# Optimization experiments

Measured on AMD Instinct MI355X. Metric: run time of the kernel, lower is better.

Reference implementation:

```python
import jax, jax.numpy as jnp
import numpy as np

NUM_CIRCLES = 7
B, D_IN, D_HID, D_OUT = 4096, 2048, 3584, 2048  # D_HID % 7 == 0 (7 * 512)


def setup_inputs() -> dict:
    key = jax.random.key(0)
    k1, k2, k3, k4 = jax.random.split(key, 4)
    x = jax.random.normal(k1, (B, D_IN), dtype=jnp.float32)
    # FlowerOfLife: 7 bias-free Linear(D_IN -> D_HID//7) weights, stacked [7, D_HID//7, D_IN]
    W_flower = jax.random.normal(k2, (NUM_CIRCLES, D_HID // NUM_CIRCLES, D_IN), dtype=jnp.float32) / np.sqrt(D_IN).astype(np.float32)
    # Merkaba: two bias-free Linear(D_HID -> D_OUT)
    W_male = jax.random.normal(k3, (D_OUT, D_HID), dtype=jnp.float32) / np.sqrt(D_HID).astype(np.float32)
    W_female = jax.random.normal(k4, (D_OUT, D_HID), dtype=jnp.float32) / np.sqrt(D_HID).astype(np.float32)
    return {"x": x, "W_flower": W_flower, "W_male": W_male, "W_female": W_female}


def reference(x, W_flower, W_male, W_female):
    # --- VesicaPiscisOperation: sacred overlap with the batch-rolled neighbor ---
    x2 = jnp.roll(x, 1, axis=0)
    dist = jnp.linalg.norm(x - x2, axis=1, keepdims=True)          # [B, 1]
    overlap = jax.nn.relu(1.0 - jnp.abs(dist - 1.0))               # [B, 1]
    x_overlap = x * (1.0 + overlap)                                # per-row scaling

    # --- FlowerOfLifeProjection: 7 parallel projections, phase-shift first 2 dims ---
    circ = jnp.einsum('bd,cod->bco', x_overlap, W_flower)          # [B, 7, D_HID//7]
    phases = 2.0 * jnp.pi * jnp.arange(NUM_CIRCLES, dtype=jnp.float32) / NUM_CIRCLES
    phase_shift = jnp.stack([jnp.cos(phases), jnp.sin(phases)], axis=-1)  # [7, 2]
    circ = circ.at[:, :, :2].multiply(phase_shift[None, :, :])
    x_expanded = circ.reshape(x.shape[0], -1)                      # [B, D_HID]

    # --- MerkabaRotation: counter-rotating transforms + sigmoid phase lock ---
    male = x_expanded @ W_male.T                                   # [B, D_OUT]
    female = x_expanded[:, ::-1] @ W_female.T                      # flip(-1) then Linear
    phase_lock = jax.nn.sigmoid(jnp.sum(male * female, axis=-1, keepdims=True))
    return phase_lock * male + (1.0 - phase_lock) * female
```

## Files before the change

### kernel.cpp

```cpp
#include <hip/hip_runtime.h>
#include <hip/hip_bf16.h>
#include <math.h>

#define B_DIM 4096
#define D_IN  2048
#define D_HID 3584
#define D_OUT 2048

typedef __bf16 bf16;
typedef float  floatx4 __attribute__((ext_vector_type(4)));
typedef bf16   bf16x8  __attribute__((ext_vector_type(8)));
typedef bf16   bf16x4  __attribute__((ext_vector_type(4)));

typedef __attribute__((address_space(1))) const void* gptr1;
typedef __attribute__((address_space(3))) void*       lptr3;

__device__ __forceinline__ void load_lds16(const void* g, void* l) {
    __builtin_amdgcn_global_load_lds((gptr1)g, (lptr3)l, 16, 0, 0);
}

struct HL { bf16 h, l; };
__device__ __forceinline__ HL split2(float v) {
    HL r;
    r.h = (bf16)v;
    r.l = (bf16)(v - (float)r.h);
    return r;
}

__global__ __launch_bounds__(256) void vesica_kernel(const float* __restrict__ x,
                                                     bf16* __restrict__ xh,
                                                     bf16* __restrict__ xl) {
    const int b  = blockIdx.x;
    const int bp = (b == 0) ? (B_DIM - 1) : (b - 1);
    const int t  = threadIdx.x;

    const floatx4* xr = (const floatx4*)(x + (size_t)b  * D_IN);
    const floatx4* pr = (const floatx4*)(x + (size_t)bp * D_IN);
    const floatx4 v0 = xr[t * 2], v1 = xr[t * 2 + 1];
    const floatx4 p0 = pr[t * 2], p1 = pr[t * 2 + 1];

    float s = 0.f;
#pragma unroll
    for (int j = 0; j < 4; ++j) {
        const float d0 = v0[j] - p0[j], d1 = v1[j] - p1[j];
        s += d0 * d0 + d1 * d1;
    }
#pragma unroll
    for (int off = 32; off > 0; off >>= 1) s += __shfl_down(s, off, 64);

    __shared__ float red[4];
    const int wave = t >> 6, lane = t & 63;
    if (lane == 0) red[wave] = s;
    __syncthreads();
    const float dist = sqrtf(red[0] + red[1] + red[2] + red[3]);
    const float sc   = 1.f + fmaxf(0.f, 1.f - fabsf(dist - 1.f));

    bf16x8 h, l;
#pragma unroll
    for (int j = 0; j < 4; ++j) {
        const HL a  = split2(v0[j] * sc);
        const HL b2 = split2(v1[j] * sc);
        h[j] = a.h;      l[j] = a.l;
        h[4 + j] = b2.h; l[4 + j] = b2.l;
    }
    ((bf16x8*)(xh + (size_t)b * D_IN))[t] = h;
    ((bf16x8*)(xl + (size_t)b * D_IN))[t] = l;
}

__global__ __launch_bounds__(256) void split_kernel(const float* __restrict__ w,
                                                    bf16* __restrict__ wh,
                                                    bf16* __restrict__ wl) {
    const size_t i = (size_t)blockIdx.x * 256 + threadIdx.x;
    const floatx4 a = ((const floatx4*)w)[i * 2];
    const floatx4 b = ((const floatx4*)w)[i * 2 + 1];
    bf16x8 h, l;
#pragma unroll
    for (int j = 0; j < 4; ++j) {
        const HL u = split2(a[j]);
        const HL v = split2(b[j]);
        h[j] = u.h;     l[j] = u.l;
        h[4 + j] = v.h; l[4 + j] = v.l;
    }
    ((bf16x8*)wh)[i] = h;
    ((bf16x8*)wl)[i] = l;
}

__global__ __launch_bounds__(256) void flipsplit_kernel(const float* __restrict__ w,
                                                        bf16* __restrict__ wh,
                                                        bf16* __restrict__ wl) {
    const int i = blockIdx.x * 256 + threadIdx.x;
    const int o = i / 448;
    const int g = i - o * 448;
    const float* src = w + (size_t)o * 3584 + (size_t)(447 - g) * 8;
    const floatx4 a = ((const floatx4*)src)[0];
    const floatx4 b = ((const floatx4*)src)[1];
    bf16x8 h, l;
#pragma unroll
    for (int j = 0; j < 4; ++j) {
        const HL u = split2(b[3 - j]);
        const HL v = split2(a[3 - j]);
        h[j] = u.h;     l[j] = u.l;
        h[4 + j] = v.h; l[4 + j] = v.l;
    }
    ((bf16x8*)wh)[(size_t)o * 448 + g] = h;
    ((bf16x8*)wl)[(size_t)o * 448 + g] = l;
}

__global__ __launch_bounds__(256) void tsplit_kernel(const float* __restrict__ w,
                                                     bf16* __restrict__ th,
                                                     bf16* __restrict__ tl) {
    __shared__ float tile[64][65];
    const int d0 = blockIdx.x * 64;
    const int h0 = blockIdx.y * 64;
    const int t  = threadIdx.x;
    const int r  = t >> 4;
    const int cg = (t & 15) << 2;

#pragma unroll
    for (int i = 0; i < 4; ++i) {
        const int hr = r + i * 16;
        const floatx4 v = *(const floatx4*)&w[(size_t)(h0 + hr) * 2048 + d0 + cg];
        tile[hr][cg]     = v[0];
        tile[hr][cg + 1] = v[1];
        tile[hr][cg + 2] = v[2];
        tile[hr][cg + 3] = v[3];
    }
    __syncthreads();

    float pm[4];
#pragma unroll
    for (int j = 0; j < 4; ++j) {
        const int h  = h0 + cg + j;
        const int hm = h & 511;
        float p = 1.f;
        if (hm < 2) {
            const float ph = 0.8975979010256552f * (float)(h >> 9);
            p = (hm == 0) ? cosf(ph) : sinf(ph);
        }
        pm[j] = p;
    }

#pragma unroll
    for (int i = 0; i < 4; ++i) {
        const int dr = r + i * 16;
        bf16x4 hh, ll;
#pragma unroll
        for (int j = 0; j < 4; ++j) {
            const HL u = split2(tile[cg + j][dr] * pm[j]);
            hh[j] = u.h;
            ll[j] = u.l;
        }
        const size_t o = (size_t)(d0 + dr) * 3584 + h0 + cg;
        *(bf16x4*)&th[o] = hh;
        *(bf16x4*)&tl[o] = ll;
    }
}

__global__ __launch_bounds__(256, 2) void gemm3_single(const bf16* __restrict__ Ah,
                                                       const bf16* __restrict__ Al,
                                                       const bf16* __restrict__ Bh,
                                                       const bf16* __restrict__ Bl,
                                                       bf16* __restrict__ C0,
                                                       bf16* __restrict__ C1,
                                                       int M, int N, int K) {
    __shared__ bf16 sAh[128 * 64], sAl[128 * 64];
    __shared__ bf16 sBh[128 * 64], sBl[128 * 64];

    const int tid  = threadIdx.x;
    const int wave = tid >> 6;
    const int lane = tid & 63;
    const int m0   = blockIdx.y * 128;
    const int n0   = blockIdx.x * 128;
    const int wm   = wave & 1;
    const int wn   = wave >> 1;

    floatx4 acc[4][4];
#pragma unroll
    for (int i = 0; i < 4; ++i)
#pragma unroll
        for (int j = 0; j < 4; ++j) acc[i][j] = (floatx4){0.f, 0.f, 0.f, 0.f};

    const int lr  = lane & 15;
    const int cc8 = (lane >> 4) << 3;

    for (int kt = 0; kt < K; kt += 64) {
#pragma unroll
        for (int i = 0; i < 4; ++i) {
            const int q = ((i * 4 + wave) << 6) + lane;
            const int r = q >> 3, c = q & 7, e = q << 3;
            const size_t ga = (size_t)(m0 + r) * K + kt + c * 8;
            const size_t gb = (size_t)(n0 + r) * K + kt + c * 8;
            load_lds16(&Ah[ga], &sAh[e]);
            load_lds16(&Al[ga], &sAl[e]);
            load_lds16(&Bh[gb], &sBh[e]);
            load_lds16(&Bl[gb], &sBl[e]);
        }
        __syncthreads();

#pragma unroll
        for (int ks = 0; ks < 2; ++ks) {
            const int ko = (ks << 5) + cc8;
            bf16x8 ah[4], al[4], bh[4], bl[4];
#pragma unroll
            for (int mi = 0; mi < 4; ++mi) {
                const int off = ((wm * 64 + mi * 16 + lr) << 6) + ko;
                ah[mi] = *(const bf16x8*)&sAh[off];
                al[mi] = *(const bf16x8*)&sAl[off];
            }
#pragma unroll
            for (int ni = 0; ni < 4; ++ni) {
                const int off = ((wn * 64 + ni * 16 + lr) << 6) + ko;
                bh[ni] = *(const bf16x8*)&sBh[off];
                bl[ni] = *(const bf16x8*)&sBl[off];
            }

#pragma unroll
            for (int mi = 0; mi < 4; ++mi)
#pragma unroll
                for (int ni = 0; ni < 4; ++ni) {
                    acc[mi][ni] = __builtin_amdgcn_mfma_f32_16x16x32_bf16(
                        ah[mi], bh[ni], acc[mi][ni], 0, 0, 0);
                    acc[mi][ni] = __builtin_amdgcn_mfma_f32_16x16x32_bf16(
                        al[mi], bh[ni], acc[mi][ni], 0, 0, 0);
                    acc[mi][ni] = __builtin_amdgcn_mfma_f32_16x16x32_bf16(
                        ah[mi], bl[ni], acc[mi][ni], 0, 0, 0);
                }
        }
        __syncthreads();
    }

    const int rq = (lane >> 4) << 2;
    const int cl = lane & 15;
#pragma unroll
    for (int mi = 0; mi < 4; ++mi) {
#pragma unroll
        for (int ni = 0; ni < 4; ++ni) {
            const int col = n0 + wn * 64 + ni * 16 + cl;
#pragma unroll
            for (int r = 0; r < 4; ++r) {
                const int row = m0 + wm * 64 + mi * 16 + rq + r;
                const size_t idx = (size_t)row * N + col;
                const HL u = split2(acc[mi][ni][r]);
                C0[idx] = u.h;
                C1[idx] = u.l;
            }
        }
    }
}

__global__ __launch_bounds__(256, 2) void gemm3_dual(const bf16* __restrict__ Ah,
                                                     const bf16* __restrict__ Al,
                                                     const bf16* __restrict__ Bmh,
                                                     const bf16* __restrict__ Bml,
                                                     const bf16* __restrict__ Bfh,
                                                     const bf16* __restrict__ Bfl,
                                                     float* __restrict__ Cm,
                                                     float* __restrict__ Cf,
                                                     int M, int N, int K) {
    __shared__ bf16 sAh[4096], sAl[4096];
    __shared__ bf16 sMh[4096], sMl[4096];
    __shared__ bf16 sFh[4096], sFl[4096];

    const int tid  = threadIdx.x;
    const int wave = tid >> 6;
    const int lane = tid & 63;
    const int m0   = blockIdx.y * 128;
    const int n0   = blockIdx.x * 128;
    const int wm   = wave & 1;
    const int wn   = wave >> 1;

    floatx4 am[4][4], af[4][4];
#pragma unroll
    for (int i = 0; i < 4; ++i)
#pragma unroll
        for (int j = 0; j < 4; ++j) {
            am[i][j] = (floatx4){0.f, 0.f, 0.f, 0.f};
            af[i][j] = (floatx4){0.f, 0.f, 0.f, 0.f};
        }

    const int lr  = lane & 15;
    const int cc8 = (lane >> 4) << 3;

    for (int kt = 0; kt < K; kt += 32) {
#pragma unroll
        for (int i = 0; i < 2; ++i) {
            const int q = ((i * 4 + wave) << 6) + lane;
            const int r = q >> 2, c = q & 3, e = q << 3;
            const size_t ga = (size_t)(m0 + r) * K + kt + c * 8;
            const size_t gb = (size_t)(n0 + r) * K + kt + c * 8;
            load_lds16(&Ah[ga],  &sAh[e]);
            load_lds16(&Al[ga],  &sAl[e]);
            load_lds16(&Bmh[gb], &sMh[e]);
            load_lds16(&Bml[gb], &sMl[e]);
            load_lds16(&Bfh[gb], &sFh[e]);
            load_lds16(&Bfl[gb], &sFl[e]);
        }
        __syncthreads();

        bf16x8 ah[4], al[4];
#pragma unroll
        for (int mi = 0; mi < 4; ++mi) {
            const int off = ((wm * 64 + mi * 16 + lr) << 5) + cc8;
            ah[mi] = *(const bf16x8*)&sAh[off];
            al[mi] = *(const bf16x8*)&sAl[off];
        }
#pragma unroll
        for (int ni = 0; ni < 4; ++ni) {
            const int off = ((wn * 64 + ni * 16 + lr) << 5) + cc8;
            const bf16x8 mh = *(const bf16x8*)&sMh[off];
            const bf16x8 ml = *(const bf16x8*)&sMl[off];
            const bf16x8 fh = *(const bf16x8*)&sFh[off];
            const bf16x8 fl = *(const bf16x8*)&sFl[off];
#pragma unroll
            for (int mi = 0; mi < 4; ++mi) {
                am[mi][ni] = __builtin_amdgcn_mfma_f32_16x16x32_bf16(
                    ah[mi], mh, am[mi][ni], 0, 0, 0);
                am[mi][ni] = __builtin_amdgcn_mfma_f32_16x16x32_bf16(
                    al[mi], mh, am[mi][ni], 0, 0, 0);
                am[mi][ni] = __builtin_amdgcn_mfma_f32_16x16x32_bf16(
                    ah[mi], ml, am[mi][ni], 0, 0, 0);
                af[mi][ni] = __builtin_amdgcn_mfma_f32_16x16x32_bf16(
                    ah[mi], fh, af[mi][ni], 0, 0, 0);
                af[mi][ni] = __builtin_amdgcn_mfma_f32_16x16x32_bf16(
                    al[mi], fh, af[mi][ni], 0, 0, 0);
                af[mi][ni] = __builtin_amdgcn_mfma_f32_16x16x32_bf16(
                    ah[mi], fl, af[mi][ni], 0, 0, 0);
            }
        }
        __syncthreads();
    }

    const int rq = (lane >> 4) << 2;
    const int cl = lane & 15;
#pragma unroll
    for (int mi = 0; mi < 4; ++mi) {
#pragma unroll
        for (int ni = 0; ni < 4; ++ni) {
            const int col = n0 + wn * 64 + ni * 16 + cl;
#pragma unroll
            for (int r = 0; r < 4; ++r) {
                const int row = m0 + wm * 64 + mi * 16 + rq + r;
                const size_t idx = (size_t)row * N + col;
                Cm[idx] = am[mi][ni][r];
                Cf[idx] = af[mi][ni][r];
            }
        }
    }
}

__global__ __launch_bounds__(256) void combine_kernel(const float* __restrict__ male,
                                                      const float* __restrict__ female,
                                                      float* __restrict__ out) {
    const int b = blockIdx.x;
    const int t = threadIdx.x;

    const floatx4* m4 = (const floatx4*)(male   + (size_t)b * D_OUT);
    const floatx4* f4 = (const floatx4*)(female + (size_t)b * D_OUT);
    const floatx4 mv0 = m4[t * 2], mv1 = m4[t * 2 + 1];
    const floatx4 fv0 = f4[t * 2], fv1 = f4[t * 2 + 1];

    float s = 0.f;
#pragma unroll
    for (int j = 0; j < 4; ++j) s += mv0[j] * fv0[j] + mv1[j] * fv1[j];
#pragma unroll
    for (int off = 32; off > 0; off >>= 1) s += __shfl_down(s, off, 64);

    __shared__ float red[4];
    const int wave = t >> 6, lane = t & 63;
    if (lane == 0) red[wave] = s;
    __syncthreads();
    const float dot = red[0] + red[1] + red[2] + red[3];
    const float pl  = 1.f / (1.f + expf(-dot));

    floatx4 o0, o1;
#pragma unroll
    for (int j = 0; j < 4; ++j) {
        o0[j] = pl * mv0[j] + (1.f - pl) * fv0[j];
        o1[j] = pl * mv1[j] + (1.f - pl) * fv1[j];
    }
    floatx4* o4 = (floatx4*)(out + (size_t)b * D_OUT);
    o4[t * 2]     = o0;
    o4[t * 2 + 1] = o1;
}

extern "C" void kernel_launch(void* const* d_in, const int* in_sizes, int n_in,
                              void* d_out, int out_size, void* d_ws, size_t ws_size,
                              hipStream_t stream) {
    const float* x   = (const float*)d_in[0];
    const float* Wfl = (const float*)d_in[1];
    const float* Wm  = (const float*)d_in[2];
    const float* Wfe = (const float*)d_in[3];
    float* out = (float*)d_out;
    (void)in_sizes; (void)n_in; (void)out_size; (void)ws_size;

    char* ws = (char*)d_ws;
    bf16*  xo_hi   = (bf16*)(ws);
    bf16*  xo_lo   = (bf16*)(ws + 16777216);
    bf16*  Wc_hi   = (bf16*)(ws + 33554432);
    bf16*  Wc_lo   = (bf16*)(ws + 50331648);
    bf16*  WflT_hi = (bf16*)(ws + 67108864);
    bf16*  WflT_lo = (bf16*)(ws + 81788928);
    bf16*  Wcat_hi = (bf16*)(ws + 96468992);
    bf16*  Wcat_lo = (bf16*)(ws + 125829120);
    float* male    = (float*)(ws + 67108864);
    float* female  = (float*)(ws + 100663296);

    vesica_kernel<<<B_DIM, 256, 0, stream>>>(x, xo_hi, xo_lo);

    tsplit_kernel<<<dim3(D_IN / 64, D_HID / 64), 256, 0, stream>>>(Wfl, WflT_hi, WflT_lo);

    split_kernel<<<(D_OUT * D_HID / 8) / 256, 256, 0, stream>>>(Wm, Wcat_hi, Wcat_lo);
    flipsplit_kernel<<<(D_OUT * (D_HID / 8)) / 256, 256, 0, stream>>>(
        Wfe, Wcat_hi + (size_t)D_OUT * D_HID, Wcat_lo + (size_t)D_OUT * D_HID);

    gemm3_single<<<dim3(D_IN / 128, (2 * D_OUT) / 128), 256, 0, stream>>>(
        Wcat_hi, Wcat_lo, WflT_hi, WflT_lo, Wc_hi, Wc_lo,
        2 * D_OUT, D_IN, D_HID);

    gemm3_dual<<<dim3(D_OUT / 128, B_DIM / 128), 256, 0, stream>>>(
        xo_hi, xo_lo,
        Wc_hi, Wc_lo,
        Wc_hi + (size_t)D_OUT * D_IN, Wc_lo + (size_t)D_OUT * D_IN,
        male, female, B_DIM, D_OUT, D_IN);

    combine_kernel<<<B_DIM, 256, 0, stream>>>(male, female, out);
}
```

Before: 510.2 us.

## Double-buffer LDS, swizzle layout, and enlarge GEMM tiles to 256x128 with 512 threads

Both split-bf16 GEMM kernels now double-buffer their LDS tiles, issuing the next K-slice's global-to-LDS loads before computing the current one. This needs only one barrier per iteration and is meant to overlap memory latency with MFMA work. The shared-memory layout gets an XOR swizzle to cut bank conflicts on the fragment reads. Blocks grow to 512 threads covering 256x128 output tiles for more reuse per load. The cost is much larger LDS use (the dual kernel needs about 128KB), which may limit occupancy, and fewer blocks in the grid.

```diff
diff --git a/kernel.cpp b/kernel.cpp
--- a/kernel.cpp
+++ b/kernel.cpp
@@ -156,23 +156,23 @@
     }
 }
 
-__global__ __launch_bounds__(256, 2) void gemm3_single(const bf16* __restrict__ Ah,
+__global__ __launch_bounds__(512, 2) void gemm3_single(const bf16* __restrict__ Ah,
                                                        const bf16* __restrict__ Al,
                                                        const bf16* __restrict__ Bh,
                                                        const bf16* __restrict__ Bl,
                                                        bf16* __restrict__ C0,
                                                        bf16* __restrict__ C1,
                                                        int M, int N, int K) {
-    __shared__ bf16 sAh[128 * 64], sAl[128 * 64];
-    __shared__ bf16 sBh[128 * 64], sBl[128 * 64];
+    __shared__ bf16 sAh[2][8192], sAl[2][8192];
+    __shared__ bf16 sBh[2][4096], sBl[2][4096];
 
     const int tid  = threadIdx.x;
     const int wave = tid >> 6;
     const int lane = tid & 63;
-    const int m0   = blockIdx.y * 128;
+    const int m0   = blockIdx.y * 256;
     const int n0   = blockIdx.x * 128;
-    const int wm   = wave & 1;
-    const int wn   = wave >> 1;
+    const int wm   = wave >> 1;
+    const int wn   = wave & 1;
 
     floatx4 acc[4][4];
 #pragma unroll
@@ -181,52 +181,66 @@
         for (int j = 0; j < 4; ++j) acc[i][j] = (floatx4){0.f, 0.f, 0.f, 0.f};
 
     const int lr  = lane & 15;
-    const int cc8 = (lane >> 4) << 3;
-
-    for (int kt = 0; kt < K; kt += 64) {
-#pragma unroll
-        for (int i = 0; i < 4; ++i) {
-            const int q = ((i * 4 + wave) << 6) + lane;
-            const int r = q >> 3, c = q & 7, e = q << 3;
+    const int cq  = lane >> 4;
+    const int hsw = (lr >> 1) & 7;
+
+    auto stage = [&](int kt, int bsel) {
+#pragma unroll
+        for (int i = 0; i < 2; ++i) {
+            const int q = (i << 9) + tid;
+            const int p = q ^ ((q >> 3) & 7);
+            const int r = p >> 2, c = p & 3;
             const size_t ga = (size_t)(m0 + r) * K + kt + c * 8;
+            load_lds16(&Ah[ga], &sAh[bsel][q << 3]);
+            load_lds16(&Al[ga], &sAl[bsel][q << 3]);
+        }
+        {
+            const int q = tid;
+            const int p = q ^ ((q >> 3) & 7);
+            const int r = p >> 2, c = p & 3;
             const size_t gb = (size_t)(n0 + r) * K + kt + c * 8;
-            load_lds16(&Ah[ga], &sAh[e]);
-            load_lds16(&Al[ga], &sAl[e]);
-            load_lds16(&Bh[gb], &sBh[e]);
-            load_lds16(&Bl[gb], &sBl[e]);
-        }
+            load_lds16(&Bh[gb], &sBh[bsel][q << 3]);
+            load_lds16(&Bl[gb], &sBl[bsel][q << 3]);
+        }
+    };
+
+    stage(0, 0);
+    __syncthreads();
+
+    int buf = 0;
+    for (int kt = 0; kt < K; kt += 32) {
+        if (kt + 32 < K) stage(kt + 32, buf ^ 1);
+
+        bf16x8 ahf[4], alf[4], bhf[4], blf[4];
+#pragma unroll
+        for (int mi = 0; mi < 4; ++mi) {
+            const int row = wm * 64 + mi * 16 + lr;
+            const int off = (((row << 2) + cq) ^ hsw) << 3;
+            ahf[mi] = *(const bf16x8*)&sAh[buf][off];
+            alf[mi] = *(const bf16x8*)&sAl[buf][off];
+        }
+#pragma unroll
+        for (int ni = 0; ni < 4; ++ni) {
+            const int row = wn * 64 + ni * 16 + lr;
+            const int off = (((row << 2) + cq) ^ hsw) << 3;
+            bhf[ni] = *(const bf16x8*)&sBh[buf][off];
+            blf[ni] = *(const bf16x8*)&sBl[buf][off];
+        }
+
+#pragma unroll
+        for (int mi = 0; mi < 4; ++mi)
+#pragma unroll
+            for (int ni = 0; ni < 4; ++ni) {
+                acc[mi][ni] = __builtin_amdgcn_mfma_f32_16x16x32_bf16(
+                    ahf[mi], bhf[ni], acc[mi][ni], 0, 0, 0);
+                acc[mi][ni] = __builtin_amdgcn_mfma_f32_16x16x32_bf16(
+                    alf[mi], bhf[ni], acc[mi][ni], 0, 0, 0);
+                acc[mi][ni] = __builtin_amdgcn_mfma_f32_16x16x32_bf16(
+                    ahf[mi], blf[ni], acc[mi][ni], 0, 0, 0);
+            }
+
         __syncthreads();
-
-#pragma unroll
-        for (int ks = 0; ks < 2; ++ks) {
-            const int ko = (ks << 5) + cc8;
-            bf16x8 ah[4], al[4], bh[4], bl[4];
-#pragma unroll
-            for (int mi = 0; mi < 4; ++mi) {
-                const int off = ((wm * 64 + mi * 16 + lr) << 6) + ko;
-                ah[mi] = *(const bf16x8*)&sAh[off];
-                al[mi] = *(const bf16x8*)&sAl[off];
-            }
-#pragma unroll
-            for (int ni = 0; ni < 4; ++ni) {
-                const int off = ((wn * 64 + ni * 16 + lr) << 6) + ko;
-                bh[ni] = *(const bf16x8*)&sBh[off];
-                bl[ni] = *(const bf16x8*)&sBl[off];
-            }
-
-#pragma unroll
-            for (int mi = 0; mi < 4; ++mi)
-#pragma unroll
-                for (int ni = 0; ni < 4; ++ni) {
-                    acc[mi][ni] = __builtin_amdgcn_mfma_f32_16x16x32_bf16(
-                        ah[mi], bh[ni], acc[mi][ni], 0, 0, 0);
-                    acc[mi][ni] = __builtin_amdgcn_mfma_f32_16x16x32_bf16(
-                        al[mi], bh[ni], acc[mi][ni], 0, 0, 0);
-                    acc[mi][ni] = __builtin_amdgcn_mfma_f32_16x16x32_bf16(
-                        ah[mi], bl[ni], acc[mi][ni], 0, 0, 0);
-                }
-        }
-        __syncthreads();
+        buf ^= 1;
     }
 
     const int rq = (lane >> 4) << 2;
@@ -248,7 +262,7 @@
     }
 }
 
-__global__ __launch_bounds__(256, 2) void gemm3_dual(const bf16* __restrict__ Ah,
+__global__ __launch_bounds__(512, 2) void gemm3_dual(const bf16* __restrict__ Ah,
                                                      const bf16* __restrict__ Al,
                                                      const bf16* __restrict__ Bmh,
                                                      const bf16* __restrict__ Bml,
@@ -257,17 +271,17 @@
                                                      float* __restrict__ Cm,
                                                      float* __restrict__ Cf,
                                                      int M, int N, int K) {
-    __shared__ bf16 sAh[4096], sAl[4096];
-    __shared__ bf16 sMh[4096], sMl[4096];
-    __shared__ bf16 sFh[4096], sFl[4096];
+    __shared__ bf16 sAh[2][8192], sAl[2][8192];
+    __shared__ bf16 sMh[2][4096], sMl[2][4096];
+    __shared__ bf16 sFh[2][4096], sFl[2][4096];
 
     const int tid  = threadIdx.x;
     const int wave = tid >> 6;
     const int lane = tid & 63;
-    const int m0   = blockIdx.y * 128;
+    const int m0   = blockIdx.y * 256;
     const int n0   = blockIdx.x * 128;
-    const int wm   = wave & 1;
-    const int wn   = wave >> 1;
+    const int wm   = wave >> 1;
+    const int wn   = wave & 1;
 
     floatx4 am[4][4], af[4][4];
 #pragma unroll
@@ -279,55 +293,73 @@
         }
 
     const int lr  = lane & 15;
-    const int cc8 = (lane >> 4) << 3;
-
+    const int cq  = lane >> 4;
+    const int hsw = (lr >> 1) & 7;
+
+    auto stage = [&](int kt, int bsel) {
+#pragma unroll
+        for (int i = 0; i < 2; ++i) {
+            const int q = (i << 9) + tid;
+            const int p = q ^ ((q >> 3) & 7);
+            const int r = p >> 2, c = p & 3;
+            const size_t ga = (size_t)(m0 + r) * K + kt + c * 8;
+            load_lds16(&Ah[ga], &sAh[bsel][q << 3]);
+            load_lds16(&Al[ga], &sAl[bsel][q << 3]);
+        }
+        {
+            const int q = tid;
+            const int p = q ^ ((q >> 3) & 7);
+            const int r = p >> 2, c = p & 3;
+            const size_t gb = (size_t)(n0 + r) * K + kt + c * 8;
+            load_lds16(&Bmh[gb], &sMh[bsel][q << 3]);
+            load_lds16(&Bml[gb], &sMl[bsel][q << 3]);
+            load_lds16(&Bfh[gb], &sFh[bsel][q << 3]);
+            load_lds16(&Bfl[gb], &sFl[bsel][q << 3]);
+        }
+    };
+
+    stage(0, 0);
+    __syncthreads();
+
+    int buf = 0;
     for (int kt = 0; kt < K; kt += 32) {
-#pragma unroll
-        for (int i = 0; i < 2; ++i) {
-            const int q = ((i * 4 + wave) << 6) + lane;
-            const int r = q >> 2, c = q & 3, e = q << 3;
-            const size_t ga = (size_t)(m0 + r) * K + kt + c * 8;
-            const size_t gb = (size_t)(n0 + r) * K + kt + c * 8;
-            load_lds16(&Ah[ga],  &sAh[e]);
-            load_lds16(&Al[ga],  &sAl[e]);
-            load_lds16(&Bmh[gb], &sMh[e]);
-            load_lds16(&Bml[gb], &sMl[e]);
-            load_lds16(&Bfh[gb], &sFh[e]);
-            load_lds16(&Bfl[gb], &sFl[e]);
-        }
-        __syncthreads();
-
-        bf16x8 ah[4], al[4];
+        if (kt + 32 < K) stage(kt + 32, buf ^ 1);
+
+        bf16x8 ahf[4], alf[4];
 #pragma unroll
         for (int mi = 0; mi < 4; ++mi) {
-            const int off = ((wm * 64 + mi * 16 + lr) << 5) + cc8;
-            ah[mi] = *(const bf16x8*)&sAh[off];
-            al[mi] = *(const bf16x8*)&sAl[off];
+            const int row = wm * 64 + mi * 16 + lr;
+            const int off = (((row << 2) + cq) ^ hsw) << 3;
+            ahf[mi] = *(const bf16x8*)&sAh[buf][off];
+            alf[mi] = *(const bf16x8*)&sAl[buf][off];
         }
 #pragma unroll
         for (int ni = 0; ni < 4; ++ni) {
-            const int off = ((wn * 64 + ni * 16 + lr) << 5) + cc8;
-            const bf16x8 mh = *(const bf16x8*)&sMh[off];
-            const bf16x8 ml = *(const bf16x8*)&sMl[off];
-            const bf16x8 fh = *(const bf16x8*)&sFh[off];
-            const bf16x8 fl = *(const bf16x8*)&sFl[off];
+            const int row = wn * 64 + ni * 16 + lr;
+            const int off = (((row << 2) + cq) ^ hsw) << 3;
+            const bf16x8 mh = *(const bf16x8*)&sMh[buf][off];
+            const bf16x8 ml = *(const bf16x8*)&sMl[buf][off];
+            const bf16x8 fh = *(const bf16x8*)&sFh[buf][off];
+            const bf16x8 fl = *(const bf16x8*)&sFl[buf][off];
 #pragma unroll
             for (int mi = 0; mi < 4; ++mi) {
                 am[mi][ni] = __builtin_amdgcn_mfma_f32_16x16x32_bf16(
-                    ah[mi], mh, am[mi][ni], 0, 0, 0);
+                    ahf[mi], mh, am[mi][ni], 0, 0, 0);
                 am[mi][ni] = __builtin_amdgcn_mfma_f32_16x16x32_bf16(
-                    al[mi], mh, am[mi][ni], 0, 0, 0);
+                    alf[mi], mh, am[mi][ni], 0, 0, 0);
                 am[mi][ni] = __builtin_amdgcn_mfma_f32_16x16x32_bf16(
-                    ah[mi], ml, am[mi][ni], 0, 0, 0);
+                    ahf[mi], ml, am[mi][ni], 0, 0, 0);
                 af[mi][ni] = __builtin_amdgcn_mfma_f32_16x16x32_bf16(
-                    ah[mi], fh, af[mi][ni], 0, 0, 0);
+                    ahf[mi], fh, af[mi][ni], 0, 0, 0);
                 af[mi][ni] = __builtin_amdgcn_mfma_f32_16x16x32_bf16(
-                    al[mi], fh, af[mi][ni], 0, 0, 0);
+                    alf[mi], fh, af[mi][ni], 0, 0, 0);
                 af[mi][ni] = __builtin_amdgcn_mfma_f32_16x16x32_bf16(
-                    ah[mi], fl, af[mi][ni], 0, 0, 0);
+                    ahf[mi], fl, af[mi][ni], 0, 0, 0);
             }
         }
+
         __syncthreads();
+        buf ^= 1;
     }
 
     const int rq = (lane >> 4) << 2;
@@ -413,11 +445,11 @@
     flipsplit_kernel<<<(D_OUT * (D_HID / 8)) / 256, 256, 0, stream>>>(
         Wfe, Wcat_hi + (size_t)D_OUT * D_HID, Wcat_lo + (size_t)D_OUT * D_HID);
 
-    gemm3_single<<<dim3(D_IN / 128, (2 * D_OUT) / 128), 256, 0, stream>>>(
+    gemm3_single<<<dim3(D_IN / 128, (2 * D_OUT) / 256), 512, 0, stream>>>(
         Wcat_hi, Wcat_lo, WflT_hi, WflT_lo, Wc_hi, Wc_lo,
         2 * D_OUT, D_IN, D_HID);
 
-    gemm3_dual<<<dim3(D_OUT / 128, B_DIM / 128), 256, 0, stream>>>(
+    gemm3_dual<<<dim3(D_OUT / 128, B_DIM / 256), 512, 0, stream>>>(
         xo_hi, xo_lo,
         Wc_hi, Wc_lo,
         Wc_hi + (size_t)D_OUT * D_IN, Wc_lo + (size_t)D_OUT * D_IN,
```

Result: slower. 547.4 us (+7.3%).
